# Kernel tuning notes

Hardware: AMD Instinct MI355X
Metric: run time of the kernel (lower is better)

The kernel has to match this reference:

```python
import jax, jax.numpy as jnp
import numpy as np

B, T, F, U = 256, 512, 64, 128

def setup_inputs() -> dict:
    key = jax.random.key(0)
    ks = jax.random.split(key, 8)
    def ortho(k, n):
        a = jax.random.normal(k, (n, n), dtype=jnp.float32)
        q, _ = jnp.linalg.qr(a)
        return q.astype(jnp.float32)
    return {
        "x": jax.random.normal(ks[0], (B, T, F), dtype=jnp.float32),
        "m": jax.random.uniform(ks[1], (B, T, F), dtype=jnp.float32),
        "delta_t": jax.random.uniform(ks[2], (B, T), dtype=jnp.float32),
        "W_z": jax.random.normal(ks[3], (F, U), dtype=jnp.float32) * 0.08,
        "U_z": ortho(ks[4], U),
        "b_z": jnp.zeros((U,), jnp.float32),
        "W_r": jax.random.normal(ks[5], (F, U), dtype=jnp.float32) * 0.08,
        "U_r": ortho(ks[6], U),
        "b_r": jnp.zeros((U,), jnp.float32),
        "W_h": jax.random.normal(ks[7], (F, U), dtype=jnp.float32) * 0.08,
        "U_h": ortho(jax.random.fold_in(key, 99), U),
        "b_h": jnp.zeros((U,), jnp.float32),
        "gamma_x_decay": jnp.ones((F,), jnp.float32),
        "gamma_h_decay": jnp.ones((U,), jnp.float32),
        "mean_imputation": jnp.zeros((F,), jnp.float32),
    }

def reference(x, m, delta_t, W_z, U_z, b_z, W_r, U_r, b_r, W_h, U_h, b_h,
              gamma_x_decay, gamma_h_decay, mean_imputation):
    # delta_t: [B,T] -> [B,T,1]
    dt = delta_t[..., None]
    # input-side decay + imputation (no recurrence -> fully vectorized)
    gamma_x = jnp.exp(-jnp.maximum(0.0, gamma_x_decay) * dt)          # [B,T,F]
    x_dec = m * x + (1.0 - m) * (gamma_x * x + (1.0 - gamma_x) * mean_imputation)
    gamma_h = jnp.exp(-jnp.maximum(0.0, gamma_h_decay) * dt)          # [B,T,U]
    # precompute input projections for all timesteps
    xz = jnp.einsum('btf,fu->btu', x_dec, W_z) + b_z
    xr = jnp.einsum('btf,fu->btu', x_dec, W_r) + b_r
    xh = jnp.einsum('btf,fu->btu', x_dec, W_h) + b_h

    def step(h, inp):
        gz, az, ar, ah = inp            # gamma_h_t [B,U], projected inputs [B,U]
        h_dec = gz * h
        z = jax.nn.sigmoid(az + h_dec @ U_z)
        r = jax.nn.sigmoid(ar + h_dec @ U_r)
        h_hat = jnp.tanh(ah + (r * h_dec) @ U_h)
        h_new = (1.0 - z) * h_dec + z * h_hat
        return h_new, h_new

    h0 = jnp.zeros((x.shape[0], U_z.shape[0]), x.dtype)
    xs = (jnp.swapaxes(gamma_h, 0, 1), jnp.swapaxes(xz, 0, 1),
          jnp.swapaxes(xr, 0, 1), jnp.swapaxes(xh, 0, 1))
    _, hs = jax.lax.scan(step, h0, xs)  # [T,B,U]
    return jnp.swapaxes(hs, 0, 1)       # [B,T,U]
```

## Files before the change

kernel.cpp:

```cpp
#include <hip/hip_runtime.h>

#define B_ 256
#define T_ 512
#define F_ 64
#define U_ 128
#define LOG2E 1.4426950408889634f
#define TSC   2.8853900817779268f

typedef _Float16 h2v __attribute__((ext_vector_type(2)));
union U32H2 { unsigned u; h2v h; };

__device__ __forceinline__ float fdot2(unsigned a, unsigned b, float c) {
  U32H2 x, y; x.u = a; y.u = b;
  return __builtin_amdgcn_fdot2(x.h, y.h, c, false);
}
__device__ __forceinline__ unsigned packh2(float a, float b) {
  U32H2 r; r.h[0] = (_Float16)a; r.h[1] = (_Float16)b; return r.u;
}
__device__ __forceinline__ float dpp1(float v) {
  return __int_as_float(__builtin_amdgcn_update_dpp(0, __float_as_int(v), 0xB1, 0xF, 0xF, true));
}
__device__ __forceinline__ float dpp2(float v) {
  return __int_as_float(__builtin_amdgcn_update_dpp(0, __float_as_int(v), 0x4E, 0xF, 0xF, true));
}

#define D4(acc, Hv, Wr, o)                                        \
  acc = fdot2(Hv.x, Wr[(o)], acc);                                \
  acc = fdot2(Hv.y, Wr[(o) + 1], acc);                            \
  acc = fdot2(Hv.z, Wr[(o) + 2], acc);                            \
  acc = fdot2(Hv.w, Wr[(o) + 3], acc);

__global__ __launch_bounds__(256, 1)
__attribute__((amdgpu_waves_per_eu(1, 1)))
void grud_kernel(
    const float* __restrict__ x, const float* __restrict__ m,
    const float* __restrict__ delta_t,
    const float* __restrict__ Wz_, const float* __restrict__ Uz, const float* __restrict__ bz,
    const float* __restrict__ Wr_, const float* __restrict__ Ur, const float* __restrict__ br,
    const float* __restrict__ Wh_, const float* __restrict__ Uh, const float* __restrict__ bh,
    const float* __restrict__ gxd, const float* __restrict__ ghd,
    const float* __restrict__ mi,
    float* __restrict__ out)
{
  const int tid = threadIdx.x;
  const int b   = blockIdx.x;
  const int kg  = tid & 3;
  const int cp  = tid >> 2;
  const int c0  = 2 * cp;

  __shared__ float  s_dt[520];
  __shared__ float  s_ghv[32 * U_];
  __shared__ float  s_hist[32 * U_];
  __shared__ __align__(16) ushort s_x16[32 * F_];
  __shared__ __align__(16) ushort s_hd16[U_];
  __shared__ __align__(16) ushort s_rh16[U_];
  __shared__ float  s_negg[U_];
  __shared__ float  s_gxf[F_];
  __shared__ float  s_mi[F_];

  unsigned uz[32], ur[32], uh[32];
  unsigned wz[16], wr[16], wh[16];
#pragma unroll
  for (int j = 0; j < 16; ++j) {
    const int k0 = 32 * kg + 2 * j;
    uz[j]      = packh2(LOG2E * Uz[k0 * U_ + c0],     LOG2E * Uz[(k0 + 1) * U_ + c0]);
    uz[16 + j] = packh2(LOG2E * Uz[k0 * U_ + c0 + 1], LOG2E * Uz[(k0 + 1) * U_ + c0 + 1]);
    ur[j]      = packh2(LOG2E * Ur[k0 * U_ + c0],     LOG2E * Ur[(k0 + 1) * U_ + c0]);
    ur[16 + j] = packh2(LOG2E * Ur[k0 * U_ + c0 + 1], LOG2E * Ur[(k0 + 1) * U_ + c0 + 1]);
    uh[j]      = packh2(TSC * Uh[k0 * U_ + c0],       TSC * Uh[(k0 + 1) * U_ + c0]);
    uh[16 + j] = packh2(TSC * Uh[k0 * U_ + c0 + 1],   TSC * Uh[(k0 + 1) * U_ + c0 + 1]);
  }
#pragma unroll
  for (int j = 0; j < 8; ++j) {
    const int f0 = 16 * kg + 2 * j;
    wz[j]     = packh2(LOG2E * Wz_[f0 * U_ + c0],     LOG2E * Wz_[(f0 + 1) * U_ + c0]);
    wz[8 + j] = packh2(LOG2E * Wz_[f0 * U_ + c0 + 1], LOG2E * Wz_[(f0 + 1) * U_ + c0 + 1]);
    wr[j]     = packh2(LOG2E * Wr_[f0 * U_ + c0],     LOG2E * Wr_[(f0 + 1) * U_ + c0]);
    wr[8 + j] = packh2(LOG2E * Wr_[f0 * U_ + c0 + 1], LOG2E * Wr_[(f0 + 1) * U_ + c0 + 1]);
    wh[j]     = packh2(TSC * Wh_[f0 * U_ + c0],       TSC * Wh_[(f0 + 1) * U_ + c0]);
    wh[8 + j] = packh2(TSC * Wh_[f0 * U_ + c0 + 1],   TSC * Wh_[(f0 + 1) * U_ + c0 + 1]);
  }
  const float biasB = (kg == 0) ? LOG2E * br[c0]
                    : (kg == 1) ? LOG2E * br[c0 + 1]
                    : (kg == 2) ? LOG2E * bz[c0]
                                : LOG2E * bz[c0 + 1];
  const float biasC = (kg & 1) ? TSC * bh[c0 + 1] : TSC * bh[c0];

  {
    const float* dtb = delta_t + (size_t)b * T_;
    s_dt[tid]       = dtb[tid];
    s_dt[tid + 256] = dtb[tid + 256];
    if (tid < 8)   s_dt[512 + tid] = 0.0f;
    if (tid < U_)  { s_negg[tid] = -fmaxf(ghd[tid], 0.0f); ((unsigned*)s_hd16)[tid >> 1] = 0u; }
    if (tid < F_)  { s_gxf[tid] = -fmaxf(gxd[tid], 0.0f); s_mi[tid] = mi[tid]; }
  }
  __syncthreads();

  float hdk = 0.0f;
  float axz0 = 0.f, axz1 = 0.f, axr0 = 0.f, axr1 = 0.f, axh0 = 0.f, axh1 = 0.f;

  for (int t0 = 0; t0 < T_; t0 += 32) {
#pragma unroll
    for (int i = 0; i < 2; ++i) {
      const int e4 = tid + 256 * i;
      const int t = e4 >> 4, f0 = (e4 & 15) << 2;
      const float dtv = s_dt[t0 + t];
      const float4 xv  = *(const float4*)(x + (size_t)(b * T_ + t0 + t) * F_ + f0);
      const float4 mv  = *(const float4*)(m + (size_t)(b * T_ + t0 + t) * F_ + f0);
      const float4 gv  = *(const float4*)(s_gxf + f0);
      const float4 miv = *(const float4*)(s_mi + f0);
      float gx, d0, d1, d2, d3;
      gx = __expf(gv.x * dtv);
      d0 = fmaf(mv.x, xv.x, (1.0f - mv.x) * (gx * xv.x + (1.0f - gx) * miv.x));
      gx = __expf(gv.y * dtv);
      d1 = fmaf(mv.y, xv.y, (1.0f - mv.y) * (gx * xv.y + (1.0f - gx) * miv.y));
      gx = __expf(gv.z * dtv);
      d2 = fmaf(mv.z, xv.z, (1.0f - mv.z) * (gx * xv.z + (1.0f - gx) * miv.z));
      gx = __expf(gv.w * dtv);
      d3 = fmaf(mv.w, xv.w, (1.0f - mv.w) * (gx * xv.w + (1.0f - gx) * miv.w));
      uint2 px; px.x = packh2(d0, d1); px.y = packh2(d2, d3);
      *(uint2*)(s_x16 + 4 * e4) = px;
    }
#pragma unroll
    for (int i = 0; i < 16; ++i) {
      const int e = tid + 256 * i;
      const int t = e >> 7, cc = e & 127;
      s_ghv[e] = __expf(s_negg[cc] * s_dt[t0 + t + 1]);
    }
    __syncthreads();

    {
      const uint4* xp = (const uint4*)(s_x16 + 16 * kg);
      float a0 = 0.f, a1 = 0.f, a2 = 0.f, a3 = 0.f, a4 = 0.f, a5 = 0.f;
#pragma unroll
      for (int q = 0; q < 2; ++q) {
        const uint4 Xv = xp[q];
        D4(a0, Xv, wz, 4 * q)  D4(a1, Xv, wz, 8 + 4 * q)
        D4(a2, Xv, wr, 4 * q)  D4(a3, Xv, wr, 8 + 4 * q)
        D4(a4, Xv, wh, 4 * q)  D4(a5, Xv, wh, 8 + 4 * q)
      }
      axz0 = a0; axz1 = a1; axr0 = a2; axr1 = a3; axh0 = a4; axh1 = a5;
    }

#pragma unroll 1
    for (int tc = 0; tc < 32; ++tc) {
      const uint4* hp = (const uint4*)(s_hd16 + 32 * kg);
      float az0 = axz0, az1 = axz1, ar0 = axr0, ar1 = axr1;
#pragma unroll
      for (int j = 0; j < 4; ++j) {
        const uint4 Hv = hp[j];
        D4(az0, Hv, uz, 4 * j)  D4(az1, Hv, uz, 16 + 4 * j)
        D4(ar0, Hv, ur, 4 * j)  D4(ar1, Hv, ur, 16 + 4 * j)
      }
      const float sR = (kg & 1) ? ar1 : ar0;
      const float oR = (kg & 1) ? ar0 : ar1;
      const float sZ = (kg & 1) ? az1 : az0;
      const float oZ = (kg & 1) ? az0 : az1;
      const float Rp = sR + dpp1(oR);
      const float Zp = sZ + dpp1(oZ);
      const float s2 = (kg & 2) ? Zp : Rp;
      const float o2 = (kg & 2) ? Rp : Zp;
      const float G  = s2 + dpp2(o2);
      const float gateB = __builtin_amdgcn_rcpf(1.0f + __builtin_amdgcn_exp2f(-(G + biasB)));
      if (kg < 2) ((_Float16*)s_rh16)[c0 + kg] = (_Float16)(gateB * hdk);
      const float zk = dpp2(gateB);
      __syncthreads();

      const float ghvk = s_ghv[tc * U_ + c0 + (kg & 1)];
      const uint4* rp = (const uint4*)(s_rh16 + 32 * kg);
      float ah0 = axh0, ah1 = axh1;
#pragma unroll
      for (int j = 0; j < 4; ++j) {
        const uint4 Rv = rp[j];
        D4(ah0, Rv, uh, 4 * j)  D4(ah1, Rv, uh, 16 + 4 * j)
      }
      if (tc < 31) {
        const uint4* xp = (const uint4*)(s_x16 + (tc + 1) * F_ + 16 * kg);
        float a0 = 0.f, a1 = 0.f, a2 = 0.f, a3 = 0.f, a4 = 0.f, a5 = 0.f;
#pragma unroll
        for (int q = 0; q < 2; ++q) {
          const uint4 Xv = xp[q];
          D4(a0, Xv, wz, 4 * q)  D4(a1, Xv, wz, 8 + 4 * q)
          D4(a2, Xv, wr, 4 * q)  D4(a3, Xv, wr, 8 + 4 * q)
          D4(a4, Xv, wh, 4 * q)  D4(a5, Xv, wh, 8 + 4 * q)
        }
        axz0 = a0; axz1 = a1; axr0 = a2; axr1 = a3; axh0 = a4; axh1 = a5;
      }
      const float sH = (kg & 1) ? ah1 : ah0;
      const float oH = (kg & 1) ? ah0 : ah1;
      const float Hp = sH + dpp1(oH);
      const float Hf = Hp + dpp2(Hp);
      const float hh = fmaf(-2.0f,
          __builtin_amdgcn_rcpf(1.0f + __builtin_amdgcn_exp2f(Hf + biasC)), 1.0f);
      const float hn = fmaf(zk, hh - hdk, hdk);
      hdk = ghvk * hn;
      if (kg < 2) {
        ((_Float16*)s_hd16)[c0 + kg] = (_Float16)hdk;
        s_hist[tc * U_ + c0 + kg] = hn;
      }
      __syncthreads();
    }

    {
      const float4* h4 = (const float4*)s_hist;
      float4* o4 = (float4*)(out + (size_t)(b * T_ + t0) * U_);
#pragma unroll
      for (int i = 0; i < 4; ++i) o4[tid + 256 * i] = h4[tid + 256 * i];
    }
  }
}

extern "C" void kernel_launch(void* const* d_in, const int* in_sizes, int n_in,
                              void* d_out, int out_size, void* d_ws, size_t ws_size,
                              hipStream_t stream) {
  const float* x   = (const float*)d_in[0];
  const float* m   = (const float*)d_in[1];
  const float* dt  = (const float*)d_in[2];
  const float* Wz  = (const float*)d_in[3];
  const float* Uz  = (const float*)d_in[4];
  const float* bz  = (const float*)d_in[5];
  const float* Wr  = (const float*)d_in[6];
  const float* Ur  = (const float*)d_in[7];
  const float* br  = (const float*)d_in[8];
  const float* Wh  = (const float*)d_in[9];
  const float* Uh  = (const float*)d_in[10];
  const float* bh  = (const float*)d_in[11];
  const float* gxd = (const float*)d_in[12];
  const float* ghd = (const float*)d_in[13];
  const float* mi  = (const float*)d_in[14];

  grud_kernel<<<dim3(B_), dim3(256), 0, stream>>>(
      x, m, dt, Wz, Uz, bz, Wr, Ur, br, Wh, Uh, bh, gxd, ghd, mi, (float*)d_out);
}
```

Baseline: 328.2 us.

## Double chunk size and split next-step input projection across recurrence phases

Raises the time chunk from 32 to 64 steps, which halves the number of chunk prologues and output flushes and doubles the shared-memory buffers. Inside the recurrence, the next step's W_z/W_r input projection is moved into the first phase, ahead of the hidden-state dot products, and the W_h projection into the second phase. All shared-memory operands are loaded up front so the independent projection work can fill latency around the serial gate math. The loop is unrolled by two. The larger buffers increase LDS use and register pressure, and the last step of each chunk does redundant projection work because the next-step index is clamped.

Result: slower. 339.4 us (+3.4%).

```diff
diff --git a/kernel.cpp b/kernel.cpp
--- a/kernel.cpp
+++ b/kernel.cpp
@@ -4,6 +4,7 @@
 #define T_ 512
 #define F_ 64
 #define U_ 128
+#define CH 64
 #define LOG2E 1.4426950408889634f
 #define TSC   2.8853900817779268f
 
@@ -49,9 +50,9 @@
   const int c0  = 2 * cp;
 
   __shared__ float  s_dt[520];
-  __shared__ float  s_ghv[32 * U_];
-  __shared__ float  s_hist[32 * U_];
-  __shared__ __align__(16) ushort s_x16[32 * F_];
+  __shared__ float  s_ghv[CH * U_];
+  __shared__ float  s_hist[CH * U_];
+  __shared__ __align__(16) ushort s_x16[CH * F_];
   __shared__ __align__(16) ushort s_hd16[U_];
   __shared__ __align__(16) ushort s_rh16[U_];
   __shared__ float  s_negg[U_];
@@ -99,9 +100,9 @@
   float hdk = 0.0f;
   float axz0 = 0.f, axz1 = 0.f, axr0 = 0.f, axr1 = 0.f, axh0 = 0.f, axh1 = 0.f;
 
-  for (int t0 = 0; t0 < T_; t0 += 32) {
-#pragma unroll
-    for (int i = 0; i < 2; ++i) {
+  for (int t0 = 0; t0 < T_; t0 += CH) {
+#pragma unroll
+    for (int i = 0; i < 4; ++i) {
       const int e4 = tid + 256 * i;
       const int t = e4 >> 4, f0 = (e4 & 15) << 2;
       const float dtv = s_dt[t0 + t];
@@ -122,7 +123,7 @@
       *(uint2*)(s_x16 + 4 * e4) = px;
     }
 #pragma unroll
-    for (int i = 0; i < 16; ++i) {
+    for (int i = 0; i < 32; ++i) {
       const int e = tid + 256 * i;
       const int t = e >> 7, cc = e & 127;
       s_ghv[e] = __expf(s_negg[cc] * s_dt[t0 + t + 1]);
@@ -142,16 +143,31 @@
       axz0 = a0; axz1 = a1; axr0 = a2; axr1 = a3; axh0 = a4; axh1 = a5;
     }
 
-#pragma unroll 1
-    for (int tc = 0; tc < 32; ++tc) {
+#pragma unroll 2
+    for (int tc = 0; tc < CH; ++tc) {
+      const int tn = (tc + 1 < CH) ? tc + 1 : tc;
+
+      const uint4* xp = (const uint4*)(s_x16 + tn * F_ + 16 * kg);
+      const uint4 X0 = xp[0], X1 = xp[1];
       const uint4* hp = (const uint4*)(s_hd16 + 32 * kg);
+      const uint4 H0 = hp[0], H1 = hp[1], H2 = hp[2], H3 = hp[3];
       float az0 = axz0, az1 = axz1, ar0 = axr0, ar1 = axr1;
-#pragma unroll
-      for (int j = 0; j < 4; ++j) {
-        const uint4 Hv = hp[j];
-        D4(az0, Hv, uz, 4 * j)  D4(az1, Hv, uz, 16 + 4 * j)
-        D4(ar0, Hv, ur, 4 * j)  D4(ar1, Hv, ur, 16 + 4 * j)
-      }
+      {
+        float a0 = 0.f, a1 = 0.f, a2 = 0.f, a3 = 0.f;
+        D4(a0, X0, wz, 0)  D4(a0, X1, wz, 4)
+        D4(a1, X0, wz, 8)  D4(a1, X1, wz, 12)
+        D4(a2, X0, wr, 0)  D4(a2, X1, wr, 4)
+        D4(a3, X0, wr, 8)  D4(a3, X1, wr, 12)
+        axz0 = a0; axz1 = a1; axr0 = a2; axr1 = a3;
+      }
+      D4(az0, H0, uz, 0)   D4(az1, H0, uz, 16)
+      D4(ar0, H0, ur, 0)   D4(ar1, H0, ur, 16)
+      D4(az0, H1, uz, 4)   D4(az1, H1, uz, 20)
+      D4(ar0, H1, ur, 4)   D4(ar1, H1, ur, 20)
+      D4(az0, H2, uz, 8)   D4(az1, H2, uz, 24)
+      D4(ar0, H2, ur, 8)   D4(ar1, H2, ur, 24)
+      D4(az0, H3, uz, 12)  D4(az1, H3, uz, 28)
+      D4(ar0, H3, ur, 12)  D4(ar1, H3, ur, 28)
       const float sR = (kg & 1) ? ar1 : ar0;
       const float oR = (kg & 1) ? ar0 : ar1;
       const float sZ = (kg & 1) ? az1 : az0;
@@ -166,26 +182,21 @@
       const float zk = dpp2(gateB);
       __syncthreads();
 
+      const uint4 Xc0 = xp[0], Xc1 = xp[1];
+      const uint4* rp = (const uint4*)(s_rh16 + 32 * kg);
+      const uint4 R0 = rp[0], R1 = rp[1], R2 = rp[2], R3 = rp[3];
       const float ghvk = s_ghv[tc * U_ + c0 + (kg & 1)];
-      const uint4* rp = (const uint4*)(s_rh16 + 32 * kg);
       float ah0 = axh0, ah1 = axh1;
-#pragma unroll
-      for (int j = 0; j < 4; ++j) {
-        const uint4 Rv = rp[j];
-        D4(ah0, Rv, uh, 4 * j)  D4(ah1, Rv, uh, 16 + 4 * j)
-      }
-      if (tc < 31) {
-        const uint4* xp = (const uint4*)(s_x16 + (tc + 1) * F_ + 16 * kg);
-        float a0 = 0.f, a1 = 0.f, a2 = 0.f, a3 = 0.f, a4 = 0.f, a5 = 0.f;
-#pragma unroll
-        for (int q = 0; q < 2; ++q) {
-          const uint4 Xv = xp[q];
-          D4(a0, Xv, wz, 4 * q)  D4(a1, Xv, wz, 8 + 4 * q)
-          D4(a2, Xv, wr, 4 * q)  D4(a3, Xv, wr, 8 + 4 * q)
-          D4(a4, Xv, wh, 4 * q)  D4(a5, Xv, wh, 8 + 4 * q)
-        }
-        axz0 = a0; axz1 = a1; axr0 = a2; axr1 = a3; axh0 = a4; axh1 = a5;
-      }
+      {
+        float a4 = 0.f, a5 = 0.f;
+        D4(a4, Xc0, wh, 0)  D4(a4, Xc1, wh, 4)
+        D4(a5, Xc0, wh, 8)  D4(a5, Xc1, wh, 12)
+        axh0 = a4; axh1 = a5;
+      }
+      D4(ah0, R0, uh, 0)   D4(ah1, R0, uh, 16)
+      D4(ah0, R1, uh, 4)   D4(ah1, R1, uh, 20)
+      D4(ah0, R2, uh, 8)   D4(ah1, R2, uh, 24)
+      D4(ah0, R3, uh, 12)  D4(ah1, R3, uh, 28)
       const float sH = (kg & 1) ? ah1 : ah0;
       const float oH = (kg & 1) ? ah0 : ah1;
       const float Hp = sH + dpp1(oH);
@@ -205,7 +216,7 @@
       const float4* h4 = (const float4*)s_hist;
       float4* o4 = (float4*)(out + (size_t)(b * T_ + t0) * U_);
 #pragma unroll
-      for (int i = 0; i < 4; ++i) o4[tid + 256 * i] = h4[tid + 256 * i];
+      for (int i = 0; i < 8; ++i) o4[tid + 256 * i] = h4[tid + 256 * i];
     }
   }
 }
```
